# Kernel optimization log

Measured on AMD Instinct MI355X. Metric: run time of the kernel, lower is better.

The kernel has to match this reference:

```python
import jax, jax.numpy as jnp
import numpy as np

B, S, D = 2, 2048, 2048
H = 16
Q_LORA, KV_LORA = 1536, 512
D_NOPE, D_ROPE = 128, 64
D_QK = D_NOPE + D_ROPE  # 192
D_V = 128
EPS = 1e-6
SCALE = D_QK ** -0.5


def rms_norm(x, w):
    var = jnp.mean(jnp.square(x), axis=-1, keepdims=True)
    return x * jax.lax.rsqrt(var + EPS) * w


def apply_rotary_emb(x, freqs_cis):
    # x: [B, S, h, dr]; freqs_cis: [S, dr//2, 2] (cos, sin); interleaved pairs
    b, s, h, dr = x.shape
    xp = x.reshape(b, s, h, dr // 2, 2)
    x0, x1 = xp[..., 0], xp[..., 1]
    cos = freqs_cis[None, :, None, :, 0]
    sin = freqs_cis[None, :, None, :, 1]
    o0 = x0 * cos - x1 * sin
    o1 = x0 * sin + x1 * cos
    return jnp.stack([o0, o1], axis=-1).reshape(b, s, h, dr)


def setup_inputs() -> dict:
    key = jax.random.key(0)
    ks = jax.random.split(key, 8)
    std = 0.02
    x = jax.random.normal(ks[0], (B, S, D), jnp.float32)
    inv_freq = 1.0 / (10000.0 ** (np.arange(0, D_ROPE, 2, dtype=np.float32) / D_ROPE))
    ang = np.outer(np.arange(S, dtype=np.float32), inv_freq)  # [S, 32]
    freqs_cis = jnp.asarray(np.stack([np.cos(ang), np.sin(ang)], axis=-1))
    return {
        'x': x,
        'freqs_cis': freqs_cis,
        'Wqa': jax.random.normal(ks[1], (Q_LORA, D), jnp.float32) * std,
        'q_a_ln_w': jnp.ones((Q_LORA,), jnp.float32),
        'Wqb': jax.random.normal(ks[2], (H * D_QK, Q_LORA), jnp.float32) * std,
        'Wkva': jax.random.normal(ks[3], (KV_LORA + D_ROPE, D), jnp.float32) * std,
        'kv_a_ln_w': jnp.ones((KV_LORA,), jnp.float32),
        'Wkvb': jax.random.normal(ks[4], (H * (D_NOPE + D_V), KV_LORA), jnp.float32) * std,
        'Wo': jax.random.normal(ks[5], (D, H * D_V), jnp.float32) * std,
    }


def reference(x, freqs_cis, Wqa, q_a_ln_w, Wqb, Wkva, kv_a_ln_w, Wkvb, Wo):
    # Low-rank Q projection: down -> RMSNorm -> up
    q = rms_norm(jnp.einsum('bsd,rd->bsr', x, Wqa), q_a_ln_w)
    q = jnp.einsum('bsr,er->bse', q, Wqb).reshape(B, S, H, D_QK)
    q_nope, q_pe = q[..., :D_NOPE], q[..., D_NOPE:]
    q = jnp.concatenate([q_nope, apply_rotary_emb(q_pe, freqs_cis)], axis=-1)

    # Low-rank KV projection with shared (MQA) rope part
    kv = jnp.einsum('bsd,ed->bse', x, Wkva)
    kv_c, k_pe = kv[..., :KV_LORA], kv[..., KV_LORA:]
    kv_c = rms_norm(kv_c, kv_a_ln_w)
    k_pe = apply_rotary_emb(k_pe[:, :, None, :], freqs_cis)  # [B,S,1,D_ROPE]
    kv = jnp.einsum('bsr,er->bse', kv_c, Wkvb).reshape(B, S, H, D_NOPE + D_V)
    k_nope, v = kv[..., :D_NOPE], kv[..., D_NOPE:]
    k = jnp.concatenate(
        [k_nope, jnp.broadcast_to(k_pe, (B, S, H, D_ROPE))], axis=-1)

    # Causal SDPA with scale = qk_head_dim ** -0.5
    scores = jnp.einsum('bqhd,bkhd->bhqk', q, k) * SCALE
    causal = jnp.tril(jnp.ones((S, S), bool))
    scores = jnp.where(causal[None, None], scores, jnp.finfo(scores.dtype).min)
    probs = jax.nn.softmax(scores, axis=-1)
    out = jnp.einsum('bhqk,bkhd->bqhd', probs, v).reshape(B, S, H * D_V)
    return jnp.einsum('bse,de->bsd', out, Wo)
```

## Files before the change

kernel.cpp:

```cpp
#include <hip/hip_runtime.h>
#include <math.h>

#define B_ 2
#define S_ 2048
#define D_ 2048
#define H_ 16
#define QLORA 1536
#define KVLORA 512
#define DN 128
#define DR 64
#define DQK 192
#define DV 128
#define EPSF 1e-6f
#define SCALEF 0.07216878364870322f

typedef short short8 __attribute__((ext_vector_type(8)));
typedef float float4v __attribute__((ext_vector_type(4)));

__device__ __forceinline__ unsigned short f2bf(float f) {
    union { float f; unsigned u; } x; x.f = f;
    unsigned r = x.u + 0x7fffu + ((x.u >> 16) & 1u);
    return (unsigned short)(r >> 16);
}
__device__ __forceinline__ float bf2f(unsigned short u) {
    union { unsigned u; float f; } x; x.u = (unsigned)u << 16;
    return x.f;
}

#define GLD16(src, dst)                                                        \
    __builtin_amdgcn_global_load_lds(                                          \
        (const __attribute__((address_space(1))) void*)(src),                  \
        (__attribute__((address_space(3))) void*)(dst), 16, 0, 0)

__global__ __launch_bounds__(256) void conv_all(
        const float* __restrict__ s0, unsigned short* __restrict__ d0, long e0,
        const float* __restrict__ s1, unsigned short* __restrict__ d1, long e1,
        const float* __restrict__ s2, unsigned short* __restrict__ d2, long e2,
        const float* __restrict__ s3, unsigned short* __restrict__ d3, long e3,
        const float* __restrict__ s4, unsigned short* __restrict__ d4, long e4,
        const float* __restrict__ s5, unsigned short* __restrict__ d5) {
    long c = (long)blockIdx.x * 256 + threadIdx.x;
    const float* src;
    unsigned short* dst;
    if      (c < e0) { src = s0; dst = d0; }
    else if (c < e1) { src = s1; dst = d1; c -= e0; }
    else if (c < e2) { src = s2; dst = d2; c -= e1; }
    else if (c < e3) { src = s3; dst = d3; c -= e2; }
    else if (c < e4) { src = s4; dst = d4; c -= e3; }
    else             { src = s5; dst = d5; c -= e4; }
    const float* p = src + c * 8;
    float4 a = *(const float4*)(p);
    float4 b = *(const float4*)(p + 4);
    union { short8 v; unsigned short u[8]; } t;
    t.u[0] = f2bf(a.x); t.u[1] = f2bf(a.y); t.u[2] = f2bf(a.z); t.u[3] = f2bf(a.w);
    t.u[4] = f2bf(b.x); t.u[5] = f2bf(b.y); t.u[6] = f2bf(b.z); t.u[7] = f2bf(b.w);
    *(short8*)&dst[c * 8] = t.v;
}

#define TBM 256
#define TBK 64

template <int MODE, int BN>
__global__ __launch_bounds__(512, 2) void gemm8(const unsigned short* __restrict__ A,
                                                const unsigned short* __restrict__ W,
                                                void* __restrict__ Cp,
                                                unsigned short* __restrict__ Cs,
                                                int M, int N, int K) {
    constexpr int NWCH = BN / 64;
    constexpr int MF = (BN == 256) ? 8 : 4;
    __shared__ unsigned short As[2][TBM * TBK];
    __shared__ unsigned short Ws[2][BN * TBK];

    const int tid = threadIdx.x;
    const int w = tid >> 6, lane = tid & 63;
    const int l16 = lane & 15, quad = lane >> 4;
    const int wm = (BN == 256) ? (w >> 2) * 128 : (w >> 1) * 64;
    const int wn = (BN == 256) ? (w & 3) * 64 : (w & 1) * 64;
    const int row0 = blockIdx.y * TBM, col0 = blockIdx.x * BN;
    const int NT = K / TBK;

    auto stage = [&](int t_, int bufi) {
        const int k0 = t_ * TBK;
#pragma unroll
        for (int i_ = 0; i_ < 4; ++i_) {
            const int ch = i_ * 512 + w * 64 + lane;
            const int r_ = ch >> 3, c_ = ch & 7;
            GLD16(&A[(size_t)(row0 + r_) * K + k0 + ((c_ ^ (r_ & 7)) << 3)],
                  &As[bufi][(i_ * 512 + w * 64) * 8]);
        }
#pragma unroll
        for (int i_ = 0; i_ < NWCH; ++i_) {
            const int ch = i_ * 512 + w * 64 + lane;
            const int r_ = ch >> 3, c_ = ch & 7;
            GLD16(&W[(size_t)(col0 + r_) * K + k0 + ((c_ ^ (r_ & 7)) << 3)],
                  &Ws[bufi][(i_ * 512 + w * 64) * 8]);
        }
    };

    const float4v zf = {0.f, 0.f, 0.f, 0.f};
    float4v acc[MF][4];
#pragma unroll
    for (int mi = 0; mi < MF; ++mi)
#pragma unroll
        for (int ni = 0; ni < 4; ++ni) acc[mi][ni] = zf;

    stage(0, 0);
    stage(1, 1);
    if constexpr (BN == 256) asm volatile("s_waitcnt vmcnt(8)" ::: "memory");
    else                     asm volatile("s_waitcnt vmcnt(6)" ::: "memory");
    __builtin_amdgcn_sched_barrier(0);
    __builtin_amdgcn_s_barrier();
    __builtin_amdgcn_sched_barrier(0);

    for (int t = 0; t < NT; ++t) {
        const int buf = t & 1;
        const unsigned short* Ab = As[buf];
        const unsigned short* Wb = Ws[buf];

        short8 bfr[2][4];
#pragma unroll
        for (int kk = 0; kk < 2; ++kk)
#pragma unroll
            for (int ni = 0; ni < 4; ++ni) {
                const int Rn = wn + ni * 16 + l16;
                bfr[kk][ni] = *(const short8*)&Wb[Rn * TBK + (((kk * 4 + quad) ^ (l16 & 7)) << 3)];
            }
#pragma unroll
        for (int mi = 0; mi < MF; ++mi) {
            const int Rm = wm + mi * 16 + l16;
            short8 a0 = *(const short8*)&Ab[Rm * TBK + (((0 + quad) ^ (l16 & 7)) << 3)];
            short8 a1 = *(const short8*)&Ab[Rm * TBK + (((4 + quad) ^ (l16 & 7)) << 3)];
#pragma unroll
            for (int ni = 0; ni < 4; ++ni) {
                acc[mi][ni] = __builtin_amdgcn_mfma_f32_16x16x32_bf16(a0, bfr[0][ni], acc[mi][ni], 0, 0, 0);
                acc[mi][ni] = __builtin_amdgcn_mfma_f32_16x16x32_bf16(a1, bfr[1][ni], acc[mi][ni], 0, 0, 0);
            }
        }

        __builtin_amdgcn_s_barrier();
        if (t + 2 < NT) {
            stage(t + 2, buf);
            if constexpr (BN == 256) asm volatile("s_waitcnt vmcnt(8)" ::: "memory");
            else                     asm volatile("s_waitcnt vmcnt(6)" ::: "memory");
        } else if (t + 1 < NT) {
            asm volatile("s_waitcnt vmcnt(0)" ::: "memory");
        }
        __builtin_amdgcn_sched_barrier(0);
        __builtin_amdgcn_s_barrier();
        __builtin_amdgcn_sched_barrier(0);
    }

    if constexpr (MODE != 2) {
#pragma unroll
        for (int mi = 0; mi < MF; ++mi)
#pragma unroll
            for (int ni = 0; ni < 4; ++ni)
#pragma unroll
                for (int r = 0; r < 4; ++r) {
                    const int row = row0 + wm + mi * 16 + quad * 4 + r;
                    const int col = col0 + wn + ni * 16 + l16;
                    if constexpr (MODE == 0)
                        ((float*)Cp)[(size_t)row * N + col] = acc[mi][ni][r];
                    else
                        ((unsigned short*)Cp)[(size_t)row * N + col] = f2bf(acc[mi][ni][r]);
                }
    } else {
        const int h = blockIdx.x;
        const int b = row0 >> 11, s0 = row0 & (S_ - 1);
        char* Tb = (char*)&As[0][0];
        if (wn < 128) {
#pragma unroll
            for (int mi = 0; mi < MF; ++mi)
#pragma unroll
                for (int ni = 0; ni < 4; ++ni)
#pragma unroll
                    for (int r = 0; r < 4; ++r) {
                        const int sl = wm + mi * 16 + quad * 4 + r;
                        const int d = wn + ni * 16 + l16;
                        Cs[((size_t)(b * H_ + h) * S_ + s0 + sl) * DQK + d] = f2bf(acc[mi][ni][r]);
                    }
        } else {
#pragma unroll
            for (int mi = 0; mi < MF; ++mi)
#pragma unroll
                for (int ni = 0; ni < 4; ++ni) {
                    const int dv = wn - 128 + ni * 16 + l16;
                    const int sl = wm + mi * 16 + quad * 4;
                    union { unsigned short u[4]; uint2 v; } pk;
                    pk.u[0] = f2bf(acc[mi][ni][0]);
                    pk.u[1] = f2bf(acc[mi][ni][1]);
                    pk.u[2] = f2bf(acc[mi][ni][2]);
                    pk.u[3] = f2bf(acc[mi][ni][3]);
                    *(uint2*)(Tb + dv * 512 + ((sl * 2) ^ ((dv & 7) << 4))) = pk.v;
                }
        }
        __syncthreads();
        unsigned short* VtP = (unsigned short*)Cp;
#pragma unroll
        for (int i = 0; i < 8; ++i) {
            const int idx = i * 512 + tid;
            const int dv = idx >> 5, sc = idx & 31;
            short8 v = *(const short8*)(Tb + dv * 512 + ((sc * 16) ^ ((dv & 7) << 4)));
            *(short8*)&VtP[((size_t)((b * H_ + h) * DV + dv)) * S_ + s0 + sc * 8] = v;
        }
    }
}

__global__ __launch_bounds__(256) void norms_fused(
        const unsigned short* __restrict__ Xb,
        const float* __restrict__ qlw,
        const float* __restrict__ kvw,
        const float* __restrict__ fc,
        unsigned short* __restrict__ qlatb,
        unsigned short* __restrict__ kvcb,
        unsigned short* __restrict__ Kbf) {
    __shared__ float tmp[4];
    int row = blockIdx.x;
    const int tid = threadIdx.x;
    const bool isq = row < (B_ * S_);
    if (!isq) row -= B_ * S_;
    const unsigned short* xrow = Xb + (size_t)row * 2176 + (isq ? 0 : QLORA);
    const int nch = isq ? 192 : 64;
    const int n = isq ? QLORA : KVLORA;

    union { short8 v; unsigned short u[8]; } t;
    float ss = 0.f;
    if (tid < nch) {
        t.v = *(const short8*)&xrow[tid * 8];
#pragma unroll
        for (int e = 0; e < 8; ++e) { float f = bf2f(t.u[e]); ss = fmaf(f, f, ss); }
    }
#pragma unroll
    for (int off = 32; off; off >>= 1) ss += __shfl_xor(ss, off, 64);
    if ((tid & 63) == 0) tmp[tid >> 6] = ss;
    __syncthreads();
    ss = tmp[0] + tmp[1] + tmp[2] + tmp[3];
    const float r = rsqrtf(ss / (float)n + EPSF);

    if (tid < nch) {
        const float* wp = (isq ? qlw : kvw) + tid * 8;
        union { short8 v; unsigned short u[8]; } o;
#pragma unroll
        for (int e = 0; e < 8; ++e) o.u[e] = f2bf(bf2f(t.u[e]) * r * wp[e]);
        if (isq) *(short8*)&qlatb[(size_t)row * QLORA + tid * 8] = o.v;
        else     *(short8*)&kvcb[(size_t)row * KVLORA + tid * 8] = o.v;
    }

    if (!isq && tid >= 64 && tid < 96) {
        const int i = tid - 64;
        const int s = row & (S_ - 1), b = row >> 11;
        float c0 = fc[(s * 32 + i) * 2 + 0];
        float s0 = fc[(s * 32 + i) * 2 + 1];
        float x0 = bf2f(xrow[KVLORA + 2 * i]);
        float x1 = bf2f(xrow[KVLORA + 2 * i + 1]);
        unsigned pk = (unsigned)f2bf(x0 * c0 - x1 * s0) |
                      ((unsigned)f2bf(x0 * s0 + x1 * c0) << 16);
#pragma unroll
        for (int h = 0; h < H_; ++h)
            *(unsigned*)&Kbf[((size_t)(b * H_ + h) * S_ + s) * DQK + DN + 2 * i] = pk;
    }
}

#define QTILES 16
#define PROW 76

__global__ __launch_bounds__(512, 1) void flash_mfma(const unsigned short* __restrict__ Qb,
                                                     const float* __restrict__ fc,
                                                     const unsigned short* __restrict__ Kbf,
                                                     const unsigned short* __restrict__ Vt,
                                                     unsigned short* __restrict__ Ob) {
    __shared__ unsigned short Ks[3][64 * 192];
    __shared__ unsigned short Vs[3][128 * 64];
    __shared__ unsigned short Ps[8][16][PROW];

    const int bh = blockIdx.x;
    const int bx = blockIdx.y;
    const int b = bh >> 4, h = bh & 15;
    const int tid = threadIdx.x;
    const int w = tid >> 6, lane = tid & 63;
    const int l16 = lane & 15, quad = lane >> 4;
    const int sw = l16 & 7;

    const unsigned short* Kg = Kbf + (size_t)bh * S_ * DQK;
    const unsigned short* Vg = Vt + (size_t)bh * DV * S_;

    auto stage = [&](int kt_, int bufi) {
        const int kb_ = kt_ * 64;
#pragma unroll
        for (int i_ = 0; i_ < 3; ++i_) {
            int ch = (w * 3 + i_) * 64 + lane;
            int r_ = ch / 24, c_ = ch - r_ * 24;
            GLD16(&Kg[(size_t)(kb_ + r_) * DQK + ((c_ ^ (r_ & 7)) << 3)],
                  &Ks[bufi][(w * 3 + i_) * 512]);
        }
#pragma unroll
        for (int i_ = 0; i_ < 2; ++i_) {
            int ch = (w * 2 + i_) * 64 + lane;
            int r_ = ch >> 3, c_ = ch & 7;
            GLD16(&Vg[(size_t)r_ * S_ + kb_ + ((c_ ^ (r_ & 7)) << 3)],
                  &Vs[bufi][(w * 2 + i_) * 512]);
        }
    };

    for (int half = 0; half < 2; ++half) {
        const int qt = half ? (QTILES - 1 - bx) : bx;
        const int q0 = qt * 128;
        const int ntiles = 2 * qt + 2;
        const int wr0 = q0 + w * 16;

        short8 a_q[6];
        {
            const int s = wr0 + l16;
            const unsigned short* qrow = Qb + (size_t)(b * S_ + s) * (H_ * DQK) + h * DQK;
#pragma unroll
            for (int i = 0; i < 6; ++i) {
                short8 t = *(const short8*)&qrow[i * 32 + quad * 8];
                if (i >= 4) {
                    union { short8 v; unsigned short u[8]; } x; x.v = t;
#pragma unroll
                    for (int j = 0; j < 4; ++j) {
                        int ip = (i - 4) * 16 + quad * 4 + j;
                        float c0 = fc[(s * 32 + ip) * 2 + 0];
                        float s0 = fc[(s * 32 + ip) * 2 + 1];
                        float x0 = bf2f(x.u[2 * j]);
                        float x1 = bf2f(x.u[2 * j + 1]);
                        x.u[2 * j]     = f2bf(x0 * c0 - x1 * s0);
                        x.u[2 * j + 1] = f2bf(x0 * s0 + x1 * c0);
                    }
                    t = x.v;
                }
                a_q[i] = t;
            }
        }

        stage(0, 0);
        if (ntiles > 1) stage(1, 1);
        asm volatile("s_waitcnt vmcnt(5)" ::: "memory");
        __builtin_amdgcn_sched_barrier(0);
        __builtin_amdgcn_s_barrier();
        __builtin_amdgcn_sched_barrier(0);

        const float4v zf = {0.f, 0.f, 0.f, 0.f};
        float4v o_acc[8] = {zf, zf, zf, zf, zf, zf, zf, zf};
        float l_r[4] = {0.f, 0.f, 0.f, 0.f};

        int cb = 0;
        for (int kt = 0; kt < ntiles; ++kt) {
            const int kb = kt * 64;

            if (kt + 2 < ntiles) {
                int sb = cb + 2; if (sb >= 3) sb -= 3;
                stage(kt + 2, sb);
            }

            if (kb <= wr0 + 15) {
                const unsigned short* Kb_ = Ks[cb];
                const unsigned short* Vb_ = Vs[cb];

                float4v sc[4] = {zf, zf, zf, zf};
#pragma unroll
                for (int i = 0; i < 6; ++i) {
                    short8 bk[4];
#pragma unroll
                    for (int kg = 0; kg < 4; ++kg)
                        bk[kg] = *(const short8*)&Kb_[(kg * 16 + l16) * 192 + (((i * 4 + quad) ^ sw) << 3)];
#pragma unroll
                    for (int kg = 0; kg < 4; ++kg)
                        sc[kg] = __builtin_amdgcn_mfma_f32_16x16x32_bf16(a_q[i], bk[kg], sc[kg], 0, 0, 0);
                }

                const bool mneed = (kb + 63 > wr0);
#pragma unroll
                for (int kg = 0; kg < 4; ++kg) {
                    const int key = kb + kg * 16 + l16;
#pragma unroll
                    for (int r = 0; r < 4; ++r) {
                        float p = __expf(sc[kg][r] * SCALEF);
                        if (mneed && key > wr0 + quad * 4 + r) p = 0.f;
                        l_r[r] += p;
                        Ps[w][quad * 4 + r][kg * 16 + l16] = f2bf(p);
                    }
                }

#pragma unroll
                for (int kc = 0; kc < 2; ++kc) {
                    short8 pa = *(const short8*)&Ps[w][l16][kc * 32 + quad * 8];
#pragma unroll
                    for (int dvt = 0; dvt < 8; ++dvt) {
                        short8 vb = *(const short8*)&Vb_[(dvt * 16 + l16) * 64 + (((kc * 4 + quad) ^ sw) << 3)];
                        o_acc[dvt] = __builtin_amdgcn_mfma_f32_16x16x32_bf16(pa, vb, o_acc[dvt], 0, 0, 0);
                    }
                }
            }

            if (kt + 2 < ntiles) {
                asm volatile("s_waitcnt vmcnt(5)" ::: "memory");
            } else if (kt + 1 < ntiles) {
                asm volatile("s_waitcnt vmcnt(0)" ::: "memory");
            }
            __builtin_amdgcn_sched_barrier(0);
            __builtin_amdgcn_s_barrier();
            __builtin_amdgcn_sched_barrier(0);

            cb = (cb == 2) ? 0 : cb + 1;
        }

#pragma unroll
        for (int r = 0; r < 4; ++r) {
            float t = l_r[r];
            t += __shfl_xor(t, 1);
            t += __shfl_xor(t, 2);
            t += __shfl_xor(t, 4);
            t += __shfl_xor(t, 8);
            l_r[r] = t;
        }
#pragma unroll
        for (int r = 0; r < 4; ++r) {
            float inv = 1.f / l_r[r];
            int row = wr0 + quad * 4 + r;
            unsigned short* op = Ob + (size_t)(b * S_ + row) * (H_ * DV) + h * DV;
#pragma unroll
            for (int dvt = 0; dvt < 8; ++dvt)
                op[dvt * 16 + l16] = f2bf(o_acc[dvt][r] * inv);
        }
    }
}

extern "C" void kernel_launch(void* const* d_in, const int* in_sizes, int n_in,
                              void* d_out, int out_size, void* d_ws, size_t ws_size,
                              hipStream_t stream) {
    const float* x    = (const float*)d_in[0];
    const float* fc   = (const float*)d_in[1];
    const float* Wqa  = (const float*)d_in[2];
    const float* qlw  = (const float*)d_in[3];
    const float* Wqb  = (const float*)d_in[4];
    const float* Wkva = (const float*)d_in[5];
    const float* kvw  = (const float*)d_in[6];
    const float* Wkvb = (const float*)d_in[7];
    const float* Wo   = (const float*)d_in[8];
    float* out = (float*)d_out;

    const int M = B_ * S_;
    const int NQKV = QLORA + 640;
    char* wsb = (char*)d_ws;

    unsigned short* qb  = (unsigned short*)wsb;
    unsigned short* Wob = (unsigned short*)(wsb + 25165824);
    char* R2 = wsb + 50331648;
    unsigned short* qlkvb = (unsigned short*)R2;
    unsigned short* xb    = (unsigned short*)(R2 + 35651584);
    unsigned short* Wcat  = (unsigned short*)(R2 + 52428800);
    unsigned short* attnb = (unsigned short*)R2;
    unsigned short* Vt    = (unsigned short*)(R2 + 16777216);
    unsigned short* Kbf   = (unsigned short*)(R2 + 35651584);
    char* R3 = R2 + 67108864;
    unsigned short* qlatb = (unsigned short*)R3;
    unsigned short* Wqbb  = (unsigned short*)(R3 + 12582912);
    char* R4 = R3 + 25165824;
    unsigned short* kvcb  = (unsigned short*)(R4 + 1048576);
    unsigned short* Wkvbb = (unsigned short*)(R4 + 5242880);

    {
        const long e0 = 1048576;
        const long e1 = e0 + 393216;
        const long e2 = e1 + 147456;
        const long e3 = e2 + 589824;
        const long e4 = e3 + 262144;
        const long tot = e4 + 524288;
        conv_all<<<(int)(tot / 256), 256, 0, stream>>>(
            x, xb, e0,
            Wqa, Wcat, e1,
            Wkva, Wcat + (size_t)QLORA * D_, e2,
            Wqb, Wqbb, e3,
            Wkvb, Wkvbb, e4,
            Wo, Wob);
    }

    gemm8<1, 128><<<dim3(NQKV / 128, M / TBM), 512, 0, stream>>>(xb, Wcat, qlkvb, nullptr, M, NQKV, D_);

    norms_fused<<<2 * M, 256, 0, stream>>>(qlkvb, qlw, kvw, fc, qlatb, kvcb, Kbf);

    gemm8<1, 256><<<dim3(H_ * DQK / 256, M / TBM), 512, 0, stream>>>(qlatb, Wqbb, qb, nullptr, M, H_ * DQK, QLORA);

    gemm8<2, 256><<<dim3(H_ * 256 / 256, M / TBM), 512, 0, stream>>>(kvcb, Wkvbb, Vt, Kbf, M, H_ * 256, KVLORA);

    flash_mfma<<<dim3(B_ * H_, QTILES / 2), 512, 0, stream>>>(qb, fc, Kbf, Vt, attnb);

    gemm8<0, 128><<<dim3(D_ / 128, M / TBM), 512, 0, stream>>>(attnb, Wob, out, nullptr, M, D_, D_);
}
```

Before: 419.6 us.

## Overlap weight conversion with first GEMM and merge Q/KV up-projection launches

Conversion of Wqb, Wkvb and Wo to bf16 now runs in 64 extra blocks of the first projection GEMM, so it overlaps with the matmul instead of sitting in the leading conversion kernel. The separate Q up-projection and KV up-projection GEMMs are combined into one launch of 448 blocks that branch on block id. This removes a launch and fills the GPU better, since the KV GEMM alone has little work. The cost is uneven block durations within one grid (K=1536 against K=512) and conversion blocks competing with GEMM blocks for bandwidth.

```diff
diff --git a/kernel.cpp b/kernel.cpp
--- a/kernel.cpp
+++ b/kernel.cpp
@@ -32,52 +32,61 @@
         (const __attribute__((address_space(1))) void*)(src),                  \
         (__attribute__((address_space(3))) void*)(dst), 16, 0, 0)
 
-__global__ __launch_bounds__(256) void conv_all(
+__device__ __forceinline__ void conv8(const float* p, unsigned short* d) {
+    float4 a = *(const float4*)(p);
+    float4 b = *(const float4*)(p + 4);
+    union { short8 v; unsigned short u[8]; } t;
+    t.u[0] = f2bf(a.x); t.u[1] = f2bf(a.y); t.u[2] = f2bf(a.z); t.u[3] = f2bf(a.w);
+    t.u[4] = f2bf(b.x); t.u[5] = f2bf(b.y); t.u[6] = f2bf(b.z); t.u[7] = f2bf(b.w);
+    *(short8*)d = t.v;
+}
+
+__global__ __launch_bounds__(256) void conv_xa(
         const float* __restrict__ s0, unsigned short* __restrict__ d0, long e0,
         const float* __restrict__ s1, unsigned short* __restrict__ d1, long e1,
-        const float* __restrict__ s2, unsigned short* __restrict__ d2, long e2,
-        const float* __restrict__ s3, unsigned short* __restrict__ d3, long e3,
-        const float* __restrict__ s4, unsigned short* __restrict__ d4, long e4,
-        const float* __restrict__ s5, unsigned short* __restrict__ d5) {
+        const float* __restrict__ s2, unsigned short* __restrict__ d2) {
     long c = (long)blockIdx.x * 256 + threadIdx.x;
     const float* src;
     unsigned short* dst;
     if      (c < e0) { src = s0; dst = d0; }
     else if (c < e1) { src = s1; dst = d1; c -= e0; }
-    else if (c < e2) { src = s2; dst = d2; c -= e1; }
-    else if (c < e3) { src = s3; dst = d3; c -= e2; }
-    else if (c < e4) { src = s4; dst = d4; c -= e3; }
-    else             { src = s5; dst = d5; c -= e4; }
-    const float* p = src + c * 8;
-    float4 a = *(const float4*)(p);
-    float4 b = *(const float4*)(p + 4);
-    union { short8 v; unsigned short u[8]; } t;
-    t.u[0] = f2bf(a.x); t.u[1] = f2bf(a.y); t.u[2] = f2bf(a.z); t.u[3] = f2bf(a.w);
-    t.u[4] = f2bf(b.x); t.u[5] = f2bf(b.y); t.u[6] = f2bf(b.z); t.u[7] = f2bf(b.w);
-    *(short8*)&dst[c * 8] = t.v;
+    else             { src = s2; dst = d2; c -= e1; }
+    conv8(src + c * 8, dst + c * 8);
 }
 
 #define TBM 256
 #define TBK 64
 
-template <int MODE, int BN>
-__global__ __launch_bounds__(512, 2) void gemm8(const unsigned short* __restrict__ A,
-                                                const unsigned short* __restrict__ W,
-                                                void* __restrict__ Cp,
-                                                unsigned short* __restrict__ Cs,
-                                                int M, int N, int K) {
-    constexpr int NWCH = BN / 64;
-    constexpr int MF = (BN == 256) ? 8 : 4;
+__global__ __launch_bounds__(512, 2) void qlkv_conv(
+        const unsigned short* __restrict__ A,
+        const unsigned short* __restrict__ W,
+        unsigned short* __restrict__ C,
+        const float* __restrict__ Wqb, unsigned short* __restrict__ Wqbb,
+        const float* __restrict__ Wkvb, unsigned short* __restrict__ Wkvbb,
+        const float* __restrict__ Wo, unsigned short* __restrict__ Wob) {
+    const int id = blockIdx.x;
+    const int tid = threadIdx.x;
+
+    if (id >= 272) {
+        const long t1 = 589824, t2 = t1 + 262144, tot = t2 + 524288;
+        for (long c = (long)(id - 272) * 512 + tid; c < tot; c += 64L * 512) {
+            const float* s; unsigned short* d; long cc = c;
+            if      (c < t1) { s = Wqb;  d = Wqbb; }
+            else if (c < t2) { s = Wkvb; d = Wkvbb; cc -= t1; }
+            else             { s = Wo;   d = Wob;   cc -= t2; }
+            conv8(s + cc * 8, d + cc * 8);
+        }
+        return;
+    }
+
+    constexpr int N = 2176, K = 2048, NT = 32;
     __shared__ unsigned short As[2][TBM * TBK];
-    __shared__ unsigned short Ws[2][BN * TBK];
-
-    const int tid = threadIdx.x;
+    __shared__ unsigned short Ws[2][128 * TBK];
+
     const int w = tid >> 6, lane = tid & 63;
     const int l16 = lane & 15, quad = lane >> 4;
-    const int wm = (BN == 256) ? (w >> 2) * 128 : (w >> 1) * 64;
-    const int wn = (BN == 256) ? (w & 3) * 64 : (w & 1) * 64;
-    const int row0 = blockIdx.y * TBM, col0 = blockIdx.x * BN;
-    const int NT = K / TBK;
+    const int wm = (w >> 1) * 64, wn = (w & 1) * 64;
+    const int row0 = (id / 17) * TBM, col0 = (id % 17) * 128;
 
     auto stage = [&](int t_, int bufi) {
         const int k0 = t_ * TBK;
@@ -89,7 +98,7 @@
                   &As[bufi][(i_ * 512 + w * 64) * 8]);
         }
 #pragma unroll
-        for (int i_ = 0; i_ < NWCH; ++i_) {
+        for (int i_ = 0; i_ < 2; ++i_) {
             const int ch = i_ * 512 + w * 64 + lane;
             const int r_ = ch >> 3, c_ = ch & 7;
             GLD16(&W[(size_t)(col0 + r_) * K + k0 + ((c_ ^ (r_ & 7)) << 3)],
@@ -98,16 +107,15 @@
     };
 
     const float4v zf = {0.f, 0.f, 0.f, 0.f};
-    float4v acc[MF][4];
-#pragma unroll
-    for (int mi = 0; mi < MF; ++mi)
+    float4v acc[4][4];
+#pragma unroll
+    for (int mi = 0; mi < 4; ++mi)
 #pragma unroll
         for (int ni = 0; ni < 4; ++ni) acc[mi][ni] = zf;
 
     stage(0, 0);
     stage(1, 1);
-    if constexpr (BN == 256) asm volatile("s_waitcnt vmcnt(8)" ::: "memory");
-    else                     asm volatile("s_waitcnt vmcnt(6)" ::: "memory");
+    asm volatile("s_waitcnt vmcnt(6)" ::: "memory");
     __builtin_amdgcn_sched_barrier(0);
     __builtin_amdgcn_s_barrier();
     __builtin_amdgcn_sched_barrier(0);
@@ -126,7 +134,7 @@
                 bfr[kk][ni] = *(const short8*)&Wb[Rn * TBK + (((kk * 4 + quad) ^ (l16 & 7)) << 3)];
             }
 #pragma unroll
-        for (int mi = 0; mi < MF; ++mi) {
+        for (int mi = 0; mi < 4; ++mi) {
             const int Rm = wm + mi * 16 + l16;
             short8 a0 = *(const short8*)&Ab[Rm * TBK + (((0 + quad) ^ (l16 & 7)) << 3)];
             short8 a1 = *(const short8*)&Ab[Rm * TBK + (((4 + quad) ^ (l16 & 7)) << 3)];
@@ -140,8 +148,7 @@
         __builtin_amdgcn_s_barrier();
         if (t + 2 < NT) {
             stage(t + 2, buf);
-            if constexpr (BN == 256) asm volatile("s_waitcnt vmcnt(8)" ::: "memory");
-            else                     asm volatile("s_waitcnt vmcnt(6)" ::: "memory");
+            asm volatile("s_waitcnt vmcnt(6)" ::: "memory");
         } else if (t + 1 < NT) {
             asm volatile("s_waitcnt vmcnt(0)" ::: "memory");
         }
@@ -150,38 +157,147 @@
         __builtin_amdgcn_sched_barrier(0);
     }
 
-    if constexpr (MODE != 2) {
-#pragma unroll
-        for (int mi = 0; mi < MF; ++mi)
+#pragma unroll
+    for (int mi = 0; mi < 4; ++mi)
+#pragma unroll
+        for (int ni = 0; ni < 4; ++ni)
+#pragma unroll
+            for (int r = 0; r < 4; ++r) {
+                const int row = row0 + wm + mi * 16 + quad * 4 + r;
+                const int col = col0 + wn + ni * 16 + l16;
+                C[(size_t)row * N + col] = f2bf(acc[mi][ni][r]);
+            }
+}
+
+__global__ __launch_bounds__(512, 2) void gemm_qkv(
+        const unsigned short* __restrict__ qlatb,
+        const unsigned short* __restrict__ Wqbb,
+        unsigned short* __restrict__ qb,
+        const unsigned short* __restrict__ kvcb,
+        const unsigned short* __restrict__ Wkvbb,
+        unsigned short* __restrict__ Vt,
+        unsigned short* __restrict__ Kbf) {
+    __shared__ unsigned short As[2][TBM * TBK];
+    __shared__ unsigned short Ws[2][256 * TBK];
+
+    const int id = blockIdx.x;
+    const int tid = threadIdx.x;
+    const bool isq = id < 192;
+    const unsigned short* A;
+    const unsigned short* W;
+    int N, K, row0, col0, hh = 0;
+    if (isq) {
+        A = qlatb; W = Wqbb; N = 3072; K = 1536;
+        col0 = (id % 12) * 256; row0 = (id / 12) * TBM;
+    } else {
+        const int idk = id - 192;
+        hh = idk % 16;
+        A = kvcb; W = Wkvbb; N = 4096; K = 512;
+        col0 = hh * 256; row0 = (idk / 16) * TBM;
+    }
+    const int NT = K / TBK;
+
+    const int w = tid >> 6, lane = tid & 63;
+    const int l16 = lane & 15, quad = lane >> 4;
+    const int wm = (w >> 2) * 128, wn = (w & 3) * 64;
+
+    auto stage = [&](int t_, int bufi) {
+        const int k0 = t_ * TBK;
+#pragma unroll
+        for (int i_ = 0; i_ < 4; ++i_) {
+            const int ch = i_ * 512 + w * 64 + lane;
+            const int r_ = ch >> 3, c_ = ch & 7;
+            GLD16(&A[(size_t)(row0 + r_) * K + k0 + ((c_ ^ (r_ & 7)) << 3)],
+                  &As[bufi][(i_ * 512 + w * 64) * 8]);
+        }
+#pragma unroll
+        for (int i_ = 0; i_ < 4; ++i_) {
+            const int ch = i_ * 512 + w * 64 + lane;
+            const int r_ = ch >> 3, c_ = ch & 7;
+            GLD16(&W[(size_t)(col0 + r_) * K + k0 + ((c_ ^ (r_ & 7)) << 3)],
+                  &Ws[bufi][(i_ * 512 + w * 64) * 8]);
+        }
+    };
+
+    const float4v zf = {0.f, 0.f, 0.f, 0.f};
+    float4v acc[8][4];
+#pragma unroll
+    for (int mi = 0; mi < 8; ++mi)
+#pragma unroll
+        for (int ni = 0; ni < 4; ++ni) acc[mi][ni] = zf;
+
+    stage(0, 0);
+    stage(1, 1);
+    asm volatile("s_waitcnt vmcnt(8)" ::: "memory");
+    __builtin_amdgcn_sched_barrier(0);
+    __builtin_amdgcn_s_barrier();
+    __builtin_amdgcn_sched_barrier(0);
+
+    for (int t = 0; t < NT; ++t) {
+        const int buf = t & 1;
+        const unsigned short* Ab = As[buf];
+        const unsigned short* Wb = Ws[buf];
+
+        short8 bfr[2][4];
+#pragma unroll
+        for (int kk = 0; kk < 2; ++kk)
+#pragma unroll
+            for (int ni = 0; ni < 4; ++ni) {
+                const int Rn = wn + ni * 16 + l16;
+                bfr[kk][ni] = *(const short8*)&Wb[Rn * TBK + (((kk * 4 + quad) ^ (l16 & 7)) << 3)];
+            }
+#pragma unroll
+        for (int mi = 0; mi < 8; ++mi) {
+            const int Rm = wm + mi * 16 + l16;
+            short8 a0 = *(const short8*)&Ab[Rm * TBK + (((0 + quad) ^ (l16 & 7)) << 3)];
+            short8 a1 = *(const short8*)&Ab[Rm * TBK + (((4 + quad) ^ (l16 & 7)) << 3)];
+#pragma unroll
+            for (int ni = 0; ni < 4; ++ni) {
+                acc[mi][ni] = __builtin_amdgcn_mfma_f32_16x16x32_bf16(a0, bfr[0][ni], acc[mi][ni], 0, 0, 0);
+                acc[mi][ni] = __builtin_amdgcn_mfma_f32_16x16x32_bf16(a1, bfr[1][ni], acc[mi][ni], 0, 0, 0);
+            }
+        }
+
+        __builtin_amdgcn_s_barrier();
+        if (t + 2 < NT) {
+            stage(t + 2, buf);
+            asm volatile("s_waitcnt vmcnt(8)" ::: "memory");
+        } else if (t + 1 < NT) {
+            asm volatile("s_waitcnt vmcnt(0)" ::: "memory");
+        }
+        __builtin_amdgcn_sched_barrier(0);
+        __builtin_amdgcn_s_barrier();
+        __builtin_amdgcn_sched_barrier(0);
+    }
+
+    if (isq) {
+#pragma unroll
+        for (int mi = 0; mi < 8; ++mi)
 #pragma unroll
             for (int ni = 0; ni < 4; ++ni)
 #pragma unroll
                 for (int r = 0; r < 4; ++r) {
                     const int row = row0 + wm + mi * 16 + quad * 4 + r;
                     const int col = col0 + wn + ni * 16 + l16;
-                    if constexpr (MODE == 0)
-                        ((float*)Cp)[(size_t)row * N + col] = acc[mi][ni][r];
-                    else
-                        ((unsigned short*)Cp)[(size_t)row * N + col] = f2bf(acc[mi][ni][r]);
+                    qb[(size_t)row * 3072 + col] = f2bf(acc[mi][ni][r]);
                 }
     } else {
-        const int h = blockIdx.x;
         const int b = row0 >> 11, s0 = row0 & (S_ - 1);
         char* Tb = (char*)&As[0][0];
         if (wn < 128) {
 #pragma unroll
-            for (int mi = 0; mi < MF; ++mi)
+            for (int mi = 0; mi < 8; ++mi)
 #pragma unroll
                 for (int ni = 0; ni < 4; ++ni)
 #pragma unroll
                     for (int r = 0; r < 4; ++r) {
                         const int sl = wm + mi * 16 + quad * 4 + r;
                         const int d = wn + ni * 16 + l16;
-                        Cs[((size_t)(b * H_ + h) * S_ + s0 + sl) * DQK + d] = f2bf(acc[mi][ni][r]);
+                        Kbf[((size_t)(b * H_ + hh) * S_ + s0 + sl) * DQK + d] = f2bf(acc[mi][ni][r]);
                     }
         } else {
 #pragma unroll
-            for (int mi = 0; mi < MF; ++mi)
+            for (int mi = 0; mi < 8; ++mi)
 #pragma unroll
                 for (int ni = 0; ni < 4; ++ni) {
                     const int dv = wn - 128 + ni * 16 + l16;
@@ -195,15 +311,109 @@
                 }
         }
         __syncthreads();
-        unsigned short* VtP = (unsigned short*)Cp;
 #pragma unroll
         for (int i = 0; i < 8; ++i) {
             const int idx = i * 512 + tid;
             const int dv = idx >> 5, sc = idx & 31;
             short8 v = *(const short8*)(Tb + dv * 512 + ((sc * 16) ^ ((dv & 7) << 4)));
-            *(short8*)&VtP[((size_t)((b * H_ + h) * DV + dv)) * S_ + s0 + sc * 8] = v;
-        }
-    }
+            *(short8*)&Vt[((size_t)((b * H_ + hh) * DV + dv)) * S_ + s0 + sc * 8] = v;
+        }
+    }
+}
+
+__global__ __launch_bounds__(512, 2) void gemm_out(const unsigned short* __restrict__ A,
+                                                   const unsigned short* __restrict__ W,
+                                                   float* __restrict__ C,
+                                                   int M, int N, int K) {
+    __shared__ unsigned short As[2][TBM * TBK];
+    __shared__ unsigned short Ws[2][128 * TBK];
+
+    const int tid = threadIdx.x;
+    const int w = tid >> 6, lane = tid & 63;
+    const int l16 = lane & 15, quad = lane >> 4;
+    const int wm = (w >> 1) * 64, wn = (w & 1) * 64;
+    const int row0 = blockIdx.y * TBM, col0 = blockIdx.x * 128;
+    const int NT = K / TBK;
+
+    auto stage = [&](int t_, int bufi) {
+        const int k0 = t_ * TBK;
+#pragma unroll
+        for (int i_ = 0; i_ < 4; ++i_) {
+            const int ch = i_ * 512 + w * 64 + lane;
+            const int r_ = ch >> 3, c_ = ch & 7;
+            GLD16(&A[(size_t)(row0 + r_) * K + k0 + ((c_ ^ (r_ & 7)) << 3)],
+                  &As[bufi][(i_ * 512 + w * 64) * 8]);
+        }
+#pragma unroll
+        for (int i_ = 0; i_ < 2; ++i_) {
+            const int ch = i_ * 512 + w * 64 + lane;
+            const int r_ = ch >> 3, c_ = ch & 7;
+            GLD16(&W[(size_t)(col0 + r_) * K + k0 + ((c_ ^ (r_ & 7)) << 3)],
+                  &Ws[bufi][(i_ * 512 + w * 64) * 8]);
+        }
+    };
+
+    const float4v zf = {0.f, 0.f, 0.f, 0.f};
+    float4v acc[4][4];
+#pragma unroll
+    for (int mi = 0; mi < 4; ++mi)
+#pragma unroll
+        for (int ni = 0; ni < 4; ++ni) acc[mi][ni] = zf;
+
+    stage(0, 0);
+    stage(1, 1);
+    asm volatile("s_waitcnt vmcnt(6)" ::: "memory");
+    __builtin_amdgcn_sched_barrier(0);
+    __builtin_amdgcn_s_barrier();
+    __builtin_amdgcn_sched_barrier(0);
+
+    for (int t = 0; t < NT; ++t) {
+        const int buf = t & 1;
+        const unsigned short* Ab = As[buf];
+        const unsigned short* Wb = Ws[buf];
+
+        short8 bfr[2][4];
+#pragma unroll
+        for (int kk = 0; kk < 2; ++kk)
+#pragma unroll
+            for (int ni = 0; ni < 4; ++ni) {
+                const int Rn = wn + ni * 16 + l16;
+                bfr[kk][ni] = *(const short8*)&Wb[Rn * TBK + (((kk * 4 + quad) ^ (l16 & 7)) << 3)];
+            }
+#pragma unroll
+        for (int mi = 0; mi < 4; ++mi) {
+            const int Rm = wm + mi * 16 + l16;
+            short8 a0 = *(const short8*)&Ab[Rm * TBK + (((0 + quad) ^ (l16 & 7)) << 3)];
+            short8 a1 = *(const short8*)&Ab[Rm * TBK + (((4 + quad) ^ (l16 & 7)) << 3)];
+#pragma unroll
+            for (int ni = 0; ni < 4; ++ni) {
+                acc[mi][ni] = __builtin_amdgcn_mfma_f32_16x16x32_bf16(a0, bfr[0][ni], acc[mi][ni], 0, 0, 0);
+                acc[mi][ni] = __builtin_amdgcn_mfma_f32_16x16x32_bf16(a1, bfr[1][ni], acc[mi][ni], 0, 0, 0);
+            }
+        }
+
+        __builtin_amdgcn_s_barrier();
+        if (t + 2 < NT) {
+            stage(t + 2, buf);
+            asm volatile("s_waitcnt vmcnt(6)" ::: "memory");
+        } else if (t + 1 < NT) {
+            asm volatile("s_waitcnt vmcnt(0)" ::: "memory");
+        }
+        __builtin_amdgcn_sched_barrier(0);
+        __builtin_amdgcn_s_barrier();
+        __builtin_amdgcn_sched_barrier(0);
+    }
+
+#pragma unroll
+    for (int mi = 0; mi < 4; ++mi)
+#pragma unroll
+        for (int ni = 0; ni < 4; ++ni)
+#pragma unroll
+            for (int r = 0; r < 4; ++r) {
+                const int row = row0 + wm + mi * 16 + quad * 4 + r;
+                const int col = col0 + wn + ni * 16 + l16;
+                C[(size_t)row * N + col] = acc[mi][ni][r];
+            }
 }
 
 __global__ __launch_bounds__(256) void norms_fused(
@@ -441,7 +651,6 @@
     float* out = (float*)d_out;
 
     const int M = B_ * S_;
-    const int NQKV = QLORA + 640;
     char* wsb = (char*)d_ws;
 
     unsigned short* qb  = (unsigned short*)wsb;
@@ -463,28 +672,21 @@
     {
         const long e0 = 1048576;
         const long e1 = e0 + 393216;
-        const long e2 = e1 + 147456;
-        const long e3 = e2 + 589824;
-        const long e4 = e3 + 262144;
-        const long tot = e4 + 524288;
-        conv_all<<<(int)(tot / 256), 256, 0, stream>>>(
+        const long tot = e1 + 147456;
+        conv_xa<<<(int)(tot / 256), 256, 0, stream>>>(
             x, xb, e0,
             Wqa, Wcat, e1,
-            Wkva, Wcat + (size_t)QLORA * D_, e2,
-            Wqb, Wqbb, e3,
-            Wkvb, Wkvbb, e4,
-            Wo, Wob);
-    }
-
-    gemm8<1, 128><<<dim3(NQKV / 128, M / TBM), 512, 0, stream>>>(xb, Wcat, qlkvb, nullptr, M, NQKV, D_);
+            Wkva, Wcat + (size_t)QLORA * D_);
+    }
+
+    qlkv_conv<<<336, 512, 0, stream>>>(xb, Wcat, qlkvb,
+                                       Wqb, Wqbb, Wkvb, Wkvbb, Wo, Wob);
 
     norms_fused<<<2 * M, 256, 0, stream>>>(qlkvb, qlw, kvw, fc, qlatb, kvcb, Kbf);
 
-    gemm8<1, 256><<<dim3(H_ * DQK / 256, M / TBM), 512, 0, stream>>>(qlatb, Wqbb, qb, nullptr, M, H_ * DQK, QLORA);
-
-    gemm8<2, 256><<<dim3(H_ * 256 / 256, M / TBM), 512, 0, stream>>>(kvcb, Wkvbb, Vt, Kbf, M, H_ * 256, KVLORA);
+    gemm_qkv<<<448, 512, 0, stream>>>(qlatb, Wqbb, qb, kvcb, Wkvbb, Vt, Kbf);
 
     flash_mfma<<<dim3(B_ * H_, QTILES / 2), 512, 0, stream>>>(qb, fc, Kbf, Vt, attnb);
 
-    gemm8<0, 128><<<dim3(D_ / 128, M / TBM), 512, 0, stream>>>(attnb, Wob, out, nullptr, M, D_, D_);
-}
+    gemm_out<<<dim3(D_ / 128, M / TBM), 512, 0, stream>>>(attnb, Wob, out, M, D_, D_);
+}
```

Result: faster. 401.4 us (-4.3%).
